# Performance work log

Measured on AMD Instinct MI355X. Metric: run time of the kernel, lower is better.

The kernel has to match this reference:

```python
import jax, jax.numpy as jnp
import numpy as np

EMPTY, TRUE, FALSE = 0.0, 1.0, 2.0  # MemoryVal ternary encoding

B = 2048          # batch
IN_BITS = 4096    # raw input bits
N_IN, N_ST, N_OUT = 2048, 1024, 1024
K = 14            # bits (connections) per neuron -> memory_size = 2**K
M = 2 ** K


def setup_inputs() -> dict:
    key = jax.random.key(0)
    ks = jax.random.split(key, 8)
    return {
        "input_bits": jax.random.randint(ks[0], (B, IN_BITS), 0, 2, dtype=jnp.int32),
        "state_bits": jax.random.randint(ks[1], (B, N_ST), 0, 2, dtype=jnp.int32),
        "in_conn": jax.random.randint(ks[2], (N_IN, K), 0, IN_BITS, dtype=jnp.int32),
        "in_mem": jax.random.randint(ks[3], (N_IN, M), 0, 3).astype(jnp.float32),
        "st_conn": jax.random.randint(ks[4], (N_ST, K), 0, N_IN + N_ST, dtype=jnp.int32),
        "st_mem": jax.random.randint(ks[5], (N_ST, M), 0, 3).astype(jnp.float32),
        "out_conn": jax.random.randint(ks[6], (N_OUT, K), 0, N_IN + N_ST, dtype=jnp.int32),
        "out_mem": jax.random.randint(ks[7], (N_OUT, M), 0, 3).astype(jnp.float32),
    }


def _ram_layer(bits, conn, mem):
    """bits: [B, T] 0/1; conn: [N, K] indices into T; mem: [N, 2**K] ternary."""
    k = conn.shape[1]
    g = bits[:, conn].astype(jnp.int32)                      # [B, N, K] gathered local bits
    w = (2 ** jnp.arange(k - 1, -1, -1)).astype(jnp.int32)   # MSB-first packing (matches _get_desired_bits)
    addr = jnp.sum(g * w, axis=-1)                           # [B, N] memory addresses
    vals = mem[jnp.arange(mem.shape[0])[None, :], addr]      # [B, N] per-neuron LUT lookup
    return jnp.where(vals == TRUE, 1.0, 0.0).astype(jnp.float32)  # neuron fires iff TRUE


def reference(input_bits, state_bits, in_conn, in_mem, st_conn, st_mem, out_conn, out_mem):
    h_in = _ram_layer(input_bits, in_conn, in_mem)                          # [B, N_IN]
    s_inp = jnp.concatenate([h_in, state_bits.astype(h_in.dtype)], axis=1)  # [B, N_IN+N_ST]
    s_out = _ram_layer(s_inp, st_conn, st_mem)                              # [B, N_ST]
    o_inp = jnp.concatenate([h_in, s_out], axis=1)                          # [B, N_IN+N_ST]
    return _ram_layer(o_inp, out_conn, out_mem)                             # [B, N_OUT]
```

## Files before the change

kernel.cpp:

```cpp
#include <hip/hip_runtime.h>
#include <stdint.h>

#define BATCH   2048
#define IN_BITS 4096
#define N_IN    2048
#define N_ST    1024
#define N_OUT   1024
#define KBITS   14
#define MW      512
#define SROW    96

#define IM4 8388608
#define SM4 4194304
#define OM4 4194304
#define GS  524288

typedef float f32x4 __attribute__((ext_vector_type(4)));
typedef int   i32x4 __attribute__((ext_vector_type(4)));

__global__ __launch_bounds__(256) void pack_mem_all(const float* __restrict__ im,
                                                    const float* __restrict__ sm,
                                                    const float* __restrict__ om,
                                                    uint32_t* __restrict__ im_p,
                                                    uint32_t* __restrict__ sm_p,
                                                    uint32_t* __restrict__ om_p) {
    const int t = blockIdx.x * 256 + threadIdx.x;
    const int lane = threadIdx.x & 63;
#pragma unroll
    for (int c = 0; c < 32; ++c) {
        const float* s; uint32_t* d; int cl;
        if (c < 16)      { s = im; d = im_p; cl = c; }
        else if (c < 24) { s = sm; d = sm_p; cl = c - 16; }
        else             { s = om; d = om_p; cl = c - 24; }
        const long i = (long)cl * GS + t;
        f32x4 v = __builtin_nontemporal_load((const f32x4*)s + i);
        unsigned long long b0 = __ballot(v[0] == 1.0f);
        unsigned long long b1 = __ballot(v[1] == 1.0f);
        unsigned long long b2 = __ballot(v[2] == 1.0f);
        unsigned long long b3 = __ballot(v[3] == 1.0f);
        if (lane < 8) {
            unsigned long long bj = (lane & 4) ? ((lane & 2) ? b3 : b2)
                                               : ((lane & 2) ? b1 : b0);
            uint32_t w = (lane & 1) ? (uint32_t)(bj >> 32) : (uint32_t)bj;
            d[((i >> 6) << 3) + lane] = w;
        }
    }
}

__global__ __launch_bounds__(256) void pack_input(const int* __restrict__ src,
                                                  uint32_t* __restrict__ dst) {
    const int t = blockIdx.x * 256 + threadIdx.x;
    const int lane = threadIdx.x & 63;
#pragma unroll
    for (int c = 0; c < 4; ++c) {
        const long i = (long)c * GS + t;
        i32x4 v = __builtin_nontemporal_load((const i32x4*)src + i);
        unsigned long long b0 = __ballot(v[0] == 1);
        unsigned long long b1 = __ballot(v[1] == 1);
        unsigned long long b2 = __ballot(v[2] == 1);
        unsigned long long b3 = __ballot(v[3] == 1);
        if (lane < 8) {
            unsigned long long bj = (lane & 4) ? ((lane & 2) ? b3 : b2)
                                               : ((lane & 2) ? b1 : b0);
            uint32_t w = (lane & 1) ? (uint32_t)(bj >> 32) : (uint32_t)bj;
            dst[((i >> 6) << 3) + lane] = w;
        }
    }
}

__global__ __launch_bounds__(256) void pack_state(const int4* __restrict__ src,
                                                  uint32_t* __restrict__ dst) {
    int t = blockIdx.x * 256 + threadIdx.x;
    int4 v = src[t];
    uint32_t nib = (uint32_t)(v.x == 1) | ((uint32_t)(v.y == 1) << 1) |
                   ((uint32_t)(v.z == 1) << 2) | ((uint32_t)(v.w == 1) << 3);
    int lane = threadIdx.x & 63;
    uint32_t w = nib << (4 * (lane & 7));
    w |= __shfl_xor(w, 1, 64);
    w |= __shfl_xor(w, 2, 64);
    w |= __shfl_xor(w, 4, 64);
    if ((lane & 7) == 0) {
        int g = t >> 3;
        int r = g >> 5;
        int c = g & 31;
        dst[(long)r * SROW + 64 + c] = w;
    }
}

template <int SRCW, int MODE>
__global__ __launch_bounds__(256) void ram_layer_t(const uint32_t* __restrict__ src,
                                                   const int* __restrict__ conn,
                                                   const uint32_t* __restrict__ memp,
                                                   uint32_t* __restrict__ dst0,
                                                   uint32_t* __restrict__ dst1,
                                                   float* __restrict__ fout) {
    constexpr int LSTR = SRCW + 1;
    __shared__ uint32_t lds[64 * LSTR];
    const int tid = threadIdx.x;
    const int b0 = blockIdx.y * 64;

    {
        const uint4* g = (const uint4*)(src + (long)b0 * SRCW);
        constexpr int NQ = 64 * SRCW / 4;
#pragma unroll
        for (int i = tid; i < NQ; i += 256) {
            uint4 v = g[i];
            int r = i / (SRCW / 4);
            int w = (i - r * (SRCW / 4)) * 4;
            uint32_t* p = &lds[r * LSTR + w];
            p[0] = v.x; p[1] = v.y; p[2] = v.z; p[3] = v.w;
        }
    }
    __syncthreads();

    const int lane = tid & 63;
    const int wave = __builtin_amdgcn_readfirstlane(tid >> 6);
    const int nw0 = blockIdx.x * 64 + wave * 16;
    const long b = b0 + lane;
    const uint32_t* row = lds + lane * LSTR;

    uint32_t acc = 0;
#pragma unroll 2
    for (int j = 0; j < 16; ++j) {
        const int n = nw0 + j;
        const int* cp = conn + n * KBITS;
        uint32_t addr = 0;
#pragma unroll
        for (int k = 0; k < KBITS; ++k) {
            int idx = cp[k];
            int wd, sh;
            if (SRCW == 128) {
                wd = ((idx >> 5) & ~7) | ((idx & 3) << 1) | ((idx >> 7) & 1);
                sh = (idx >> 2) & 31;
            } else {
                wd = idx >> 5;
                sh = idx & 31;
            }
            addr = (addr << 1) | ((row[wd] >> sh) & 1u);
        }
        uint32_t mw = ((addr >> 5) & ~7u) | ((addr & 3u) << 1) | ((addr >> 7) & 1u);
        uint32_t bit = (memp[(long)n * MW + mw] >> ((addr >> 2) & 31u)) & 1u;
        if (MODE == 2) {
            fout[b * N_OUT + n] = (float)bit;
        } else {
            acc |= bit << j;
        }
    }
    if (MODE != 2) {
        const int woff = (MODE == 0 ? 0 : 64) + (nw0 >> 5);
        const int half = (nw0 >> 4) & 1;
        ((ushort*)(dst0 + b * SROW + woff))[half] = (ushort)acc;
        if (MODE == 0)
            ((ushort*)(dst1 + b * SROW + woff))[half] = (ushort)acc;
    }
}

extern "C" void kernel_launch(void* const* d_in, const int* in_sizes, int n_in,
                              void* d_out, int out_size, void* d_ws, size_t ws_size,
                              hipStream_t stream) {
    const int*   input_bits = (const int*)d_in[0];
    const int*   state_bits = (const int*)d_in[1];
    const int*   in_conn    = (const int*)d_in[2];
    const float* in_mem     = (const float*)d_in[3];
    const int*   st_conn    = (const int*)d_in[4];
    const float* st_mem     = (const float*)d_in[5];
    const int*   out_conn   = (const int*)d_in[6];
    const float* out_mem    = (const float*)d_in[7];
    float*       out        = (float*)d_out;

    char* ws = (char*)d_ws;
    uint32_t* bits1 = (uint32_t*)(ws);
    uint32_t* buf_s = (uint32_t*)(ws + 1048576);
    uint32_t* buf_o = (uint32_t*)(ws + 1048576 + 786432);
    uint32_t* im_p  = (uint32_t*)(ws + 1048576 + 2 * 786432);
    uint32_t* sm_p  = (uint32_t*)(ws + 1048576 + 2 * 786432 + 4194304);
    uint32_t* om_p  = (uint32_t*)(ws + 1048576 + 2 * 786432 + 4194304 + 2097152);

    pack_input<<<2048, 256, 0, stream>>>(input_bits, bits1);
    pack_state<<<(BATCH * N_ST / 4) / 256, 256, 0, stream>>>((const int4*)state_bits, buf_s);
    pack_mem_all<<<2048, 256, 0, stream>>>(in_mem, st_mem, out_mem, im_p, sm_p, om_p);

    ram_layer_t<128, 0><<<dim3(N_IN / 64, BATCH / 64), 256, 0, stream>>>(
        bits1, in_conn, im_p, buf_s, buf_o, nullptr);
    ram_layer_t<SROW, 1><<<dim3(N_ST / 64, BATCH / 64), 256, 0, stream>>>(
        buf_s, st_conn, sm_p, buf_o, nullptr, nullptr);
    ram_layer_t<SROW, 2><<<dim3(N_OUT / 64, BATCH / 64), 256, 0, stream>>>(
        buf_o, out_conn, om_p, nullptr, nullptr, out);
}
```

Before: 339.3 us.

## Fuse packing and three RAM layers into one cooperative persistent kernel

Replaces six separate launches with a single cooperative kernel of 1024 blocks that packs memories and inputs, then runs the three RAM layers separated by grid-wide syncs. The shared-memory tile now uses an XOR swizzle instead of padding, and each block covers a different neuron/batch tiling (64 or 32 neurons per block). The output layer writes vectorised float4 results. This is meant to remove launch gaps and tail effects between kernels, at the cost of grid-sync overhead and a fixed grid size that limits occupancy. The old multi-kernel path is kept as a fallback if the cooperative launch fails.

```diff
diff --git a/kernel.cpp b/kernel.cpp
--- a/kernel.cpp
+++ b/kernel.cpp
@@ -1,4 +1,5 @@
 #include <hip/hip_runtime.h>
+#include <hip/hip_cooperative_groups.h>
 #include <stdint.h>
 
 #define BATCH   2048
@@ -14,9 +15,166 @@
 #define SM4 4194304
 #define OM4 4194304
 #define GS  524288
+#define FTH 262144
 
 typedef float f32x4 __attribute__((ext_vector_type(4)));
 typedef int   i32x4 __attribute__((ext_vector_type(4)));
+
+namespace cg = cooperative_groups;
+
+
+__device__ __forceinline__ void pack4f(const float* __restrict__ s,
+                                       uint32_t* __restrict__ d, long i, int lane) {
+    f32x4 v = __builtin_nontemporal_load((const f32x4*)s + i);
+    unsigned long long b0 = __ballot(v[0] == 1.0f);
+    unsigned long long b1 = __ballot(v[1] == 1.0f);
+    unsigned long long b2 = __ballot(v[2] == 1.0f);
+    unsigned long long b3 = __ballot(v[3] == 1.0f);
+    if (lane < 8) {
+        unsigned long long bj = (lane & 4) ? ((lane & 2) ? b3 : b2)
+                                           : ((lane & 2) ? b1 : b0);
+        uint32_t w = (lane & 1) ? (uint32_t)(bj >> 32) : (uint32_t)bj;
+        d[((i >> 6) << 3) + lane] = w;
+    }
+}
+__device__ __forceinline__ void pack4i(const int* __restrict__ s,
+                                       uint32_t* __restrict__ d, long i, int lane) {
+    i32x4 v = __builtin_nontemporal_load((const i32x4*)s + i);
+    unsigned long long b0 = __ballot(v[0] == 1);
+    unsigned long long b1 = __ballot(v[1] == 1);
+    unsigned long long b2 = __ballot(v[2] == 1);
+    unsigned long long b3 = __ballot(v[3] == 1);
+    if (lane < 8) {
+        unsigned long long bj = (lane & 4) ? ((lane & 2) ? b3 : b2)
+                                           : ((lane & 2) ? b1 : b0);
+        uint32_t w = (lane & 1) ? (uint32_t)(bj >> 32) : (uint32_t)bj;
+        d[((i >> 6) << 3) + lane] = w;
+    }
+}
+
+template <int SRCW, int NPB, int MODE>
+__device__ __forceinline__ void ram_phase(const uint32_t* __restrict__ src,
+                                          const int* __restrict__ conn,
+                                          const uint32_t* __restrict__ memp,
+                                          uint32_t* __restrict__ dst0,
+                                          uint32_t* __restrict__ dst1,
+                                          float* __restrict__ fout,
+                                          uint32_t* lds) {
+    const int tid = threadIdx.x;
+    const int bid = blockIdx.x;
+    const int ng = bid & 31;
+    const int bg = bid >> 5;
+    const int b0 = bg * 64;
+
+    {
+        const uint32_t* g = src + (long)b0 * SRCW;
+        for (int i = tid; i < 64 * SRCW; i += 256) {
+            int r = i / SRCW;
+            int w = i - r * SRCW;
+            lds[r * 128 + (w ^ (r & 31))] = g[i];
+        }
+    }
+    __syncthreads();
+
+    const int lane = tid & 63;
+    const int lx = lane & 31;
+    const int wave = __builtin_amdgcn_readfirstlane(tid >> 6);
+    constexpr int NPW = NPB / 4;
+    const int n0 = ng * NPB + wave * NPW;
+    const long b = b0 + lane;
+    const uint32_t* row = lds + lane * 128;
+
+    uint32_t acc = 0;
+#pragma unroll 4
+    for (int j = 0; j < NPW; ++j) {
+        const int n = n0 + j;
+        const int* cp = conn + n * KBITS;
+        uint32_t addr = 0;
+#pragma unroll
+        for (int k = 0; k < KBITS; ++k) {
+            int idx = cp[k];
+            int wd, sh;
+            if (SRCW == 128) {
+                wd = ((idx >> 5) & ~7) | ((idx & 3) << 1) | ((idx >> 7) & 1);
+                sh = (idx >> 2) & 31;
+            } else {
+                wd = idx >> 5;
+                sh = idx & 31;
+            }
+            addr = (addr << 1) | ((row[wd ^ lx] >> sh) & 1u);
+        }
+        uint32_t mw = ((addr >> 5) & ~7u) | ((addr & 3u) << 1) | ((addr >> 7) & 1u);
+        uint32_t bit = (memp[(long)n * MW + mw] >> ((addr >> 2) & 31u)) & 1u;
+        acc |= bit << j;
+    }
+    if (MODE == 0) {
+        const int woff = n0 >> 5;
+        const int half = (n0 >> 4) & 1;
+        ((ushort*)(dst0 + b * SROW + woff))[half] = (ushort)acc;
+        ((ushort*)(dst1 + b * SROW + woff))[half] = (ushort)acc;
+    } else if (MODE == 1) {
+        ((unsigned char*)(dst0 + b * SROW + 64))[n0 >> 3] = (unsigned char)acc;
+    } else {
+        float* op = fout + b * N_OUT + n0;
+        f32x4 fa, fb;
+#pragma unroll
+        for (int q = 0; q < 4; ++q) {
+            fa[q] = (float)((acc >> q) & 1u);
+            fb[q] = (float)((acc >> (q + 4)) & 1u);
+        }
+        *(f32x4*)op = fa;
+        *((f32x4*)op + 1) = fb;
+    }
+}
+
+__global__ __launch_bounds__(256, 4) void fused_all(
+    const int* __restrict__ input_bits, const int* __restrict__ state_bits,
+    const int* __restrict__ in_conn, const float* __restrict__ in_mem,
+    const int* __restrict__ st_conn, const float* __restrict__ st_mem,
+    const int* __restrict__ out_conn, const float* __restrict__ out_mem,
+    float* __restrict__ out,
+    uint32_t* __restrict__ bits1, uint32_t* __restrict__ buf_s,
+    uint32_t* __restrict__ buf_o, uint32_t* __restrict__ im_p,
+    uint32_t* __restrict__ sm_p, uint32_t* __restrict__ om_p) {
+    __shared__ uint32_t lds[64 * 128];
+    const int t = blockIdx.x * 256 + threadIdx.x;
+    const int lane = threadIdx.x & 63;
+
+#pragma unroll 4
+    for (int c = 0; c < 32; ++c) pack4f(in_mem, im_p, (long)c * FTH + t, lane);
+#pragma unroll 4
+    for (int c = 0; c < 16; ++c) pack4f(st_mem, sm_p, (long)c * FTH + t, lane);
+#pragma unroll 4
+    for (int c = 0; c < 16; ++c) pack4f(out_mem, om_p, (long)c * FTH + t, lane);
+#pragma unroll
+    for (int c = 0; c < 8; ++c)  pack4i(input_bits, bits1, (long)c * FTH + t, lane);
+#pragma unroll
+    for (int c = 0; c < 2; ++c) {
+        long i = (long)c * FTH + t;
+        i32x4 v = __builtin_nontemporal_load((const i32x4*)state_bits + i);
+        uint32_t nib = (uint32_t)(v[0] == 1) | ((uint32_t)(v[1] == 1) << 1) |
+                       ((uint32_t)(v[2] == 1) << 2) | ((uint32_t)(v[3] == 1) << 3);
+        uint32_t w = nib << (4 * (lane & 7));
+        w |= __shfl_xor(w, 1, 64);
+        w |= __shfl_xor(w, 2, 64);
+        w |= __shfl_xor(w, 4, 64);
+        if ((lane & 7) == 0) {
+            long g = i >> 3;
+            long r = g >> 5;
+            int  cc = (int)(g & 31);
+            buf_s[r * SROW + 64 + cc] = w;
+        }
+    }
+    cg::this_grid().sync();
+
+    ram_phase<128, 64, 0>(bits1, in_conn, im_p, buf_s, buf_o, nullptr, lds);
+    cg::this_grid().sync();
+
+    ram_phase<SROW, 32, 1>(buf_s, st_conn, sm_p, buf_o, nullptr, nullptr, lds);
+    cg::this_grid().sync();
+
+    ram_phase<SROW, 32, 2>(buf_o, out_conn, om_p, nullptr, nullptr, out, lds);
+}
 
 __global__ __launch_bounds__(256) void pack_mem_all(const float* __restrict__ im,
                                                     const float* __restrict__ sm,
@@ -32,42 +190,16 @@
         if (c < 16)      { s = im; d = im_p; cl = c; }
         else if (c < 24) { s = sm; d = sm_p; cl = c - 16; }
         else             { s = om; d = om_p; cl = c - 24; }
-        const long i = (long)cl * GS + t;
-        f32x4 v = __builtin_nontemporal_load((const f32x4*)s + i);
-        unsigned long long b0 = __ballot(v[0] == 1.0f);
-        unsigned long long b1 = __ballot(v[1] == 1.0f);
-        unsigned long long b2 = __ballot(v[2] == 1.0f);
-        unsigned long long b3 = __ballot(v[3] == 1.0f);
-        if (lane < 8) {
-            unsigned long long bj = (lane & 4) ? ((lane & 2) ? b3 : b2)
-                                               : ((lane & 2) ? b1 : b0);
-            uint32_t w = (lane & 1) ? (uint32_t)(bj >> 32) : (uint32_t)bj;
-            d[((i >> 6) << 3) + lane] = w;
-        }
-    }
-}
-
+        pack4f(s, d, (long)cl * GS + t, lane);
+    }
+}
 __global__ __launch_bounds__(256) void pack_input(const int* __restrict__ src,
                                                   uint32_t* __restrict__ dst) {
     const int t = blockIdx.x * 256 + threadIdx.x;
     const int lane = threadIdx.x & 63;
 #pragma unroll
-    for (int c = 0; c < 4; ++c) {
-        const long i = (long)c * GS + t;
-        i32x4 v = __builtin_nontemporal_load((const i32x4*)src + i);
-        unsigned long long b0 = __ballot(v[0] == 1);
-        unsigned long long b1 = __ballot(v[1] == 1);
-        unsigned long long b2 = __ballot(v[2] == 1);
-        unsigned long long b3 = __ballot(v[3] == 1);
-        if (lane < 8) {
-            unsigned long long bj = (lane & 4) ? ((lane & 2) ? b3 : b2)
-                                               : ((lane & 2) ? b1 : b0);
-            uint32_t w = (lane & 1) ? (uint32_t)(bj >> 32) : (uint32_t)bj;
-            dst[((i >> 6) << 3) + lane] = w;
-        }
-    }
-}
-
+    for (int c = 0; c < 4; ++c) pack4i(src, dst, (long)c * GS + t, lane);
+}
 __global__ __launch_bounds__(256) void pack_state(const int4* __restrict__ src,
                                                   uint32_t* __restrict__ dst) {
     int t = blockIdx.x * 256 + threadIdx.x;
@@ -81,12 +213,9 @@
     w |= __shfl_xor(w, 4, 64);
     if ((lane & 7) == 0) {
         int g = t >> 3;
-        int r = g >> 5;
-        int c = g & 31;
-        dst[(long)r * SROW + 64 + c] = w;
-    }
-}
-
+        dst[(long)(g >> 5) * SROW + 64 + (g & 31)] = w;
+    }
+}
 template <int SRCW, int MODE>
 __global__ __launch_bounds__(256) void ram_layer_t(const uint32_t* __restrict__ src,
                                                    const int* __restrict__ conn,
@@ -98,7 +227,6 @@
     __shared__ uint32_t lds[64 * LSTR];
     const int tid = threadIdx.x;
     const int b0 = blockIdx.y * 64;
-
     {
         const uint4* g = (const uint4*)(src + (long)b0 * SRCW);
         constexpr int NQ = 64 * SRCW / 4;
@@ -112,13 +240,11 @@
         }
     }
     __syncthreads();
-
     const int lane = tid & 63;
     const int wave = __builtin_amdgcn_readfirstlane(tid >> 6);
     const int nw0 = blockIdx.x * 64 + wave * 16;
     const long b = b0 + lane;
     const uint32_t* row = lds + lane * LSTR;
-
     uint32_t acc = 0;
 #pragma unroll 2
     for (int j = 0; j < 16; ++j) {
@@ -140,11 +266,8 @@
         }
         uint32_t mw = ((addr >> 5) & ~7u) | ((addr & 3u) << 1) | ((addr >> 7) & 1u);
         uint32_t bit = (memp[(long)n * MW + mw] >> ((addr >> 2) & 31u)) & 1u;
-        if (MODE == 2) {
-            fout[b * N_OUT + n] = (float)bit;
-        } else {
-            acc |= bit << j;
-        }
+        if (MODE == 2) fout[b * N_OUT + n] = (float)bit;
+        else           acc |= bit << j;
     }
     if (MODE != 2) {
         const int woff = (MODE == 0 ? 0 : 64) + (nw0 >> 5);
@@ -176,14 +299,23 @@
     uint32_t* sm_p  = (uint32_t*)(ws + 1048576 + 2 * 786432 + 4194304);
     uint32_t* om_p  = (uint32_t*)(ws + 1048576 + 2 * 786432 + 4194304 + 2097152);
 
-    pack_input<<<2048, 256, 0, stream>>>(input_bits, bits1);
-    pack_state<<<(BATCH * N_ST / 4) / 256, 256, 0, stream>>>((const int4*)state_bits, buf_s);
-    pack_mem_all<<<2048, 256, 0, stream>>>(in_mem, st_mem, out_mem, im_p, sm_p, om_p);
-
-    ram_layer_t<128, 0><<<dim3(N_IN / 64, BATCH / 64), 256, 0, stream>>>(
-        bits1, in_conn, im_p, buf_s, buf_o, nullptr);
-    ram_layer_t<SROW, 1><<<dim3(N_ST / 64, BATCH / 64), 256, 0, stream>>>(
-        buf_s, st_conn, sm_p, buf_o, nullptr, nullptr);
-    ram_layer_t<SROW, 2><<<dim3(N_OUT / 64, BATCH / 64), 256, 0, stream>>>(
-        buf_o, out_conn, om_p, nullptr, nullptr, out);
-}
+    void* kargs[] = {
+        (void*)&input_bits, (void*)&state_bits, (void*)&in_conn, (void*)&in_mem,
+        (void*)&st_conn, (void*)&st_mem, (void*)&out_conn, (void*)&out_mem,
+        (void*)&out, (void*)&bits1, (void*)&buf_s, (void*)&buf_o,
+        (void*)&im_p, (void*)&sm_p, (void*)&om_p};
+    hipError_t err = hipLaunchCooperativeKernel((const void*)fused_all,
+                                                dim3(1024), dim3(256),
+                                                kargs, 0, stream);
+    if (err != hipSuccess) {
+        pack_input<<<2048, 256, 0, stream>>>(input_bits, bits1);
+        pack_state<<<(BATCH * N_ST / 4) / 256, 256, 0, stream>>>((const int4*)state_bits, buf_s);
+        pack_mem_all<<<2048, 256, 0, stream>>>(in_mem, st_mem, out_mem, im_p, sm_p, om_p);
+        ram_layer_t<128, 0><<<dim3(N_IN / 64, BATCH / 64), 256, 0, stream>>>(
+            bits1, in_conn, im_p, buf_s, buf_o, nullptr);
+        ram_layer_t<SROW, 1><<<dim3(N_ST / 64, BATCH / 64), 256, 0, stream>>>(
+            buf_s, st_conn, sm_p, buf_o, nullptr, nullptr);
+        ram_layer_t<SROW, 2><<<dim3(N_OUT / 64, BATCH / 64), 256, 0, stream>>>(
+            buf_o, out_conn, om_p, nullptr, nullptr, out);
+    }
+}
```

New measurement: 716.5 us. +111.2%, slower.
